# Performance work log

Measured on AMD Instinct MI355X. Metric: run time of the kernel, lower is better.

## Reference

```python
import jax, jax.numpy as jnp
import numpy as np

NATOMS = 8
NSHELLS = 13  # primitives per atom
NELEC = 32
NORB = 72
NBATCH = 8192

L_PAT = [0,0,1,1,1,1,1,1,2,2,2,2,2]
M_PAT = [0,0,-1,0,1,-1,0,1,-2,-1,0,1,2]
CTR_PAT = [0,0,1,2,3,1,2,3,4,5,6,7,8]
EXP_PAT = [0.5,1.5,0.8,0.8,0.8,2.0,2.0,2.0,1.2,1.2,1.2,1.2,1.2]
COEF_PAT = [1.0,0.5,1.0,1.0,1.0,0.7,0.7,0.7,1.0,1.0,1.0,1.0,1.0]


def setup_inputs() -> dict:
    key = jax.random.key(0)
    pos = jax.random.normal(key, (NBATCH, NELEC, 3), dtype=jnp.float32) * 3.0
    atom_coords = jnp.asarray(
        np.array([[1.5 * a, 1.0 * (a % 2), 0.8 * (a % 3)] for a in range(NATOMS)],
                 dtype=np.float32))
    bas_exp = jnp.asarray(np.array(EXP_PAT * NATOMS, dtype=np.float32))
    bas_coeffs = jnp.asarray(np.array(COEF_PAT * NATOMS, dtype=np.float32))
    bas_n = jnp.asarray(np.array(L_PAT * NATOMS, dtype=np.float32))
    bas_l = jnp.asarray(np.array(L_PAT * NATOMS, dtype=np.int32))
    bas_m = jnp.asarray(np.array(M_PAT * NATOMS, dtype=np.int32))
    index_ctr = jnp.asarray(
        np.array([c + 9 * a for a in range(NATOMS) for c in CTR_PAT], dtype=np.int32))
    return dict(pos=pos, atom_coords=atom_coords, bas_exp=bas_exp,
                bas_coeffs=bas_coeffs, bas_n=bas_n, bas_l=bas_l, bas_m=bas_m,
                index_ctr=index_ctr)


def _norm_gaussian(bas_exp, bas_n):
    # N = sqrt(2 n! / (2n)! * (4 beta)^n * sqrt(beta/pi)),  beta = 2*alpha
    beta = 2.0 * bas_exp
    nfact = jnp.exp(jax.scipy.special.gammaln(bas_n + 1.0))
    twonfact = jnp.exp(jax.scipy.special.gammaln(2.0 * bas_n + 1.0))
    return jnp.sqrt(2.0 * nfact / twonfact * (4.0 * beta) ** bas_n
                    * jnp.sqrt(beta / np.pi))


def _spherical_harmonics(xyz, r2, bas_l, bas_m):
    # real spherical harmonics for l = 0, 1, 2 (QMCTorch convention)
    x, y, z = xyz[..., 0], xyz[..., 1], xyz[..., 2]
    r = jnp.sqrt(r2)
    C0 = 0.2820948  # 1/(2 sqrt(pi))
    C1 = 0.4886025119029199
    C2 = 1.0925484305920792
    C20 = 0.31539156525252005
    C22 = 0.5462742152960396
    y1 = C1 * jnp.where(bas_m == -1, y, jnp.where(bas_m == 0, z, x)) / r
    y2 = jnp.where(bas_m == -2, C2 * x * y,
         jnp.where(bas_m == -1, C2 * y * z,
         jnp.where(bas_m == 0, C20 * (2.0 * z * z - x * x - y * y),
         jnp.where(bas_m == 1, C2 * x * z, C22 * (x * x - y * y))))) / r2
    return jnp.where(bas_l == 0, C0, jnp.where(bas_l == 1, y1, y2))


def reference(pos, atom_coords, bas_exp, bas_coeffs, bas_n, bas_l, bas_m, index_ctr):
    # bas_coords: [nbas, 3] via repeat_interleave(nshells)
    bas_coords = jnp.repeat(atom_coords, NSHELLS, axis=0)
    # xyz: [B, nelec, nbas, 3]
    xyz = pos.reshape(-1, NELEC, 1, 3) - bas_coords[None, None, :, :]
    r2 = jnp.sum(xyz * xyz, axis=-1)            # [B, nelec, nbas]
    R = jnp.sqrt(r2)
    Rad = R ** bas_n * jnp.exp(-bas_exp * r2)   # gto radial: r^n exp(-a r^2)
    Y = _spherical_harmonics(xyz, r2, bas_l, bas_m)
    norm = _norm_gaussian(bas_exp, bas_n)
    bas = norm * bas_coeffs * Rad * Y           # [B, nelec, nbas]
    ao = jnp.zeros((pos.shape[0], NELEC, NORB), dtype=bas.dtype)
    ao = ao.at[:, :, index_ctr].add(bas)        # scatter-add over contractions
    return ao
```

## Files before the change

kernel.cpp:

```cpp
#include <hip/hip_runtime.h>


#define NBATCH 8192
#define NELEC 32
#define NORB 72
#define NATOMS 8
#define NROWS (NBATCH * NELEC)
#define ROWS_PER_BLOCK 64
#define THREADS 512
#define OUT_F4_PER_BLOCK (ROWS_PER_BLOCK * NORB / 4)

typedef float f4 __attribute__((ext_vector_type(4)));

__global__ __launch_bounds__(THREADS) void ao_kernel(
        const float* __restrict__ pos,
        const float* __restrict__ atom_coords,
        float* __restrict__ out)
{
    __shared__ f4 sOutV[OUT_F4_PER_BLOCK];
    float* sOut = (float*)sOutV;
    __shared__ float sPos[ROWS_PER_BLOCK * 3];
    __shared__ float sAtom[NATOMS * 3];

    const int tid = threadIdx.x;
    const int row0 = blockIdx.x * ROWS_PER_BLOCK;

    if (tid < ROWS_PER_BLOCK * 3) sPos[tid] = pos[row0 * 3 + tid];
    if (tid < NATOMS * 3)         sAtom[tid] = atom_coords[tid];
    __syncthreads();

    const int lr   = tid >> 3;
    const int atom = tid & 7;

    const float x = sPos[lr * 3 + 0] - sAtom[atom * 3 + 0];
    const float y = sPos[lr * 3 + 1] - sAtom[atom * 3 + 1];
    const float z = sPos[lr * 3 + 2] - sAtom[atom * 3 + 2];

    const float r2 = x * x + y * y + z * z;

    const float e05 = __expf(-0.5f * r2);
    const float e15 = __expf(-1.5f * r2);
    const float e08 = __expf(-0.8f * r2);
    const float e20 = __expf(-2.0f * r2);
    const float e12 = __expf(-1.2f * r2);

    const float ws = 0.29965575f * e05 + 0.19718457f * e15;
    const float wp = 1.0442109f * e08 + 1.4532531f * e20;

    const float xy = x * y, yz = y * z, xz = x * z;
    const float Aq = (x - y) * (x + y);
    const float Bq = 3.0f * z * z - r2;

    float* o = &sOut[lr * NORB + atom * 9];
    o[0] = ws;
    o[1] = wp * y;
    o[2] = wp * z;
    o[3] = wp * x;
    o[4] = 4.0031479f * xy * e12;
    o[5] = 4.0031479f * yz * e12;
    o[6] = 1.1556093f * Bq * e12;
    o[7] = 4.0031479f * xz * e12;
    o[8] = 2.0015740f * Aq * e12;
    __syncthreads();

    f4* out4 = (f4*)out;
    const int base4 = blockIdx.x * OUT_F4_PER_BLOCK;
    #pragma unroll
    for (int i = tid; i < OUT_F4_PER_BLOCK; i += THREADS)
        __builtin_nontemporal_store(sOutV[i], &out4[base4 + i]);
}

extern "C" void kernel_launch(void* const* d_in, const int* in_sizes, int n_in,
                              void* d_out, int out_size, void* d_ws, size_t ws_size,
                              hipStream_t stream) {
    const float* pos         = (const float*)d_in[0];
    const float* atom_coords = (const float*)d_in[1];
    float* out = (float*)d_out;

    const int nblocks = NROWS / ROWS_PER_BLOCK;
    ao_kernel<<<nblocks, THREADS, 0, stream>>>(pos, atom_coords, out);
}
```

Measured before the change: 101.2 us.

## Use persistent blocks with double-buffered tiles to overlap compute and stores

Launches a fixed grid of 1024 blocks, each looping over 4 tiles. Positions for the next tile are prefetched and its AO values computed into a second LDS buffer while the current buffer is stored. The nontemporal stores become plain stores. LDS use per block doubles, which may cut occupancy, and the kernel is essentially write-bandwidth bound, so any gain from overlap is probably small.

```diff
diff --git a/kernel.cpp b/kernel.cpp
--- a/kernel.cpp
+++ b/kernel.cpp
@@ -6,36 +6,25 @@
 #define NORB 72
 #define NATOMS 8
 #define NROWS (NBATCH * NELEC)
-#define ROWS_PER_BLOCK 64
+#define ROWS_PER_TILE 64
 #define THREADS 512
-#define OUT_F4_PER_BLOCK (ROWS_PER_BLOCK * NORB / 4)
+#define F4_PER_TILE (ROWS_PER_TILE * NORB / 4)
+#define NTILES (NROWS / ROWS_PER_TILE)
+#define GRID 1024
+#define TILES_PER_BLOCK (NTILES / GRID)
 
 typedef float f4 __attribute__((ext_vector_type(4)));
 
-__global__ __launch_bounds__(THREADS) void ao_kernel(
-        const float* __restrict__ pos,
-        const float* __restrict__ atom_coords,
-        float* __restrict__ out)
-{
-    __shared__ f4 sOutV[OUT_F4_PER_BLOCK];
-    float* sOut = (float*)sOutV;
-    __shared__ float sPos[ROWS_PER_BLOCK * 3];
-    __shared__ float sAtom[NATOMS * 3];
-
-    const int tid = threadIdx.x;
-    const int row0 = blockIdx.x * ROWS_PER_BLOCK;
-
-    if (tid < ROWS_PER_BLOCK * 3) sPos[tid] = pos[row0 * 3 + tid];
-    if (tid < NATOMS * 3)         sAtom[tid] = atom_coords[tid];
-    __syncthreads();
-
+__device__ __forceinline__ void compute_tile(float* __restrict__ sOut,
+                                             const float* __restrict__ sPos,
+                                             const float* __restrict__ sAtom,
+                                             int tid) {
     const int lr   = tid >> 3;
     const int atom = tid & 7;
 
     const float x = sPos[lr * 3 + 0] - sAtom[atom * 3 + 0];
     const float y = sPos[lr * 3 + 1] - sAtom[atom * 3 + 1];
     const float z = sPos[lr * 3 + 2] - sAtom[atom * 3 + 2];
-
     const float r2 = x * x + y * y + z * z;
 
     const float e05 = __expf(-0.5f * r2);
@@ -61,13 +50,43 @@
     o[6] = 1.1556093f * Bq * e12;
     o[7] = 4.0031479f * xz * e12;
     o[8] = 2.0015740f * Aq * e12;
+}
+
+__global__ __launch_bounds__(THREADS) void ao_kernel(
+        const float* __restrict__ pos,
+        const float* __restrict__ atom_coords,
+        float* __restrict__ out)
+{
+    __shared__ f4 buf[2][F4_PER_TILE];
+    __shared__ float sPos[2][ROWS_PER_TILE * 3];
+    __shared__ float sAtom[NATOMS * 3];
+
+    const int tid = threadIdx.x;
+    const int t0  = blockIdx.x;
+
+    if (tid < NATOMS * 3) sAtom[tid] = atom_coords[tid];
+    if (tid < ROWS_PER_TILE * 3)
+        sPos[0][tid] = pos[t0 * (ROWS_PER_TILE * 3) + tid];
     __syncthreads();
+    compute_tile((float*)buf[0], sPos[0], sAtom, tid);
 
     f4* out4 = (f4*)out;
-    const int base4 = blockIdx.x * OUT_F4_PER_BLOCK;
     #pragma unroll
-    for (int i = tid; i < OUT_F4_PER_BLOCK; i += THREADS)
-        __builtin_nontemporal_store(sOutV[i], &out4[base4 + i]);
+    for (int k = 0; k < TILES_PER_BLOCK; ++k) {
+        const int cur = k & 1;
+        if (k + 1 < TILES_PER_BLOCK && tid < ROWS_PER_TILE * 3)
+            sPos[cur ^ 1][tid] =
+                pos[(t0 + (k + 1) * GRID) * (ROWS_PER_TILE * 3) + tid];
+        __syncthreads();
+
+        const long base4 = (long)(t0 + k * GRID) * F4_PER_TILE;
+        #pragma unroll
+        for (int i = tid; i < F4_PER_TILE; i += THREADS)
+            out4[base4 + i] = buf[cur][i];
+
+        if (k + 1 < TILES_PER_BLOCK)
+            compute_tile((float*)buf[cur ^ 1], sPos[cur ^ 1], sAtom, tid);
+    }
 }
 
 extern "C" void kernel_launch(void* const* d_in, const int* in_sizes, int n_in,
@@ -76,7 +95,5 @@
     const float* pos         = (const float*)d_in[0];
     const float* atom_coords = (const float*)d_in[1];
     float* out = (float*)d_out;
-
-    const int nblocks = NROWS / ROWS_PER_BLOCK;
-    ao_kernel<<<nblocks, THREADS, 0, stream>>>(pos, atom_coords, out);
+    ao_kernel<<<GRID, THREADS, 0, stream>>>(pos, atom_coords, out);
 }
```

Result: no change. 99.40 us (-1.8%).
